# Optimization experiments

Measured on AMD Instinct MI355X. Metric: run time of the kernel, lower is better.

Reference implementation:

```python
import jax, jax.numpy as jnp
import numpy as np

B, N, C, H, L, FF, OUT = 8, 512, 1024, 16, 6, 4096, 2
HD = C // H
EPS = 1e-6


def _pos_encoding(n, d):
    pos = np.arange(n)[:, None].astype(np.float64)
    i = np.arange(d)[None, :].astype(np.float64)
    ang = pos / np.power(10000.0, 2 * (i // 2) / np.float32(d))
    ang[:, 0::2] = np.sin(ang[:, 0::2])
    ang[:, 1::2] = np.cos(ang[:, 1::2])
    return jnp.asarray(ang[None], dtype=jnp.float32)  # [1, N, C]


def setup_inputs() -> dict:
    key = jax.random.key(0)
    ks = jax.random.split(key, 16)
    s = 0.02
    inp = {
        'inputs': jax.random.normal(ks[0], (B, N, C), jnp.float32),
        'attention_mask': jnp.ones((B, 1, 1, N), jnp.int32),
        'pos_enc': _pos_encoding(N, C),
        'Wi': jax.random.normal(ks[1], (C, C), jnp.float32) * s,
        'bi': jnp.zeros((C,), jnp.float32),
        'ln1_g': jnp.ones((L, C), jnp.float32),
        'ln1_b': jnp.zeros((L, C), jnp.float32),
        'Wqkv': jax.random.normal(ks[2], (L, 3 * C, C), jnp.float32) * s,
        'bqkv': jnp.zeros((L, 3 * C), jnp.float32),
        'Wo': jax.random.normal(ks[3], (L, C, C), jnp.float32) * s,
        'bo': jnp.zeros((L, C), jnp.float32),
        'ln2_g': jnp.ones((L, C), jnp.float32),
        'ln2_b': jnp.zeros((L, C), jnp.float32),
        'W1': jax.random.normal(ks[4], (L, FF, C), jnp.float32) * s,
        'b1': jnp.zeros((L, FF), jnp.float32),
        'W2': jax.random.normal(ks[5], (L, C, FF), jnp.float32) * s,
        'b2': jnp.zeros((L, C), jnp.float32),
        'Wout': jax.random.normal(ks[6], (OUT, C), jnp.float32) * s,
        'bout': jnp.zeros((OUT,), jnp.float32),
    }
    return inp


def _layernorm(x, g, b):
    mu = jnp.mean(x, axis=-1, keepdims=True)
    var = jnp.mean(jnp.square(x - mu), axis=-1, keepdims=True)
    return (x - mu) * jax.lax.rsqrt(var + EPS) * g + b


def _forward(inputs, attention_mask, pos_enc, Wi, bi, ln1_g, ln1_b, Wqkv, bqkv,
             Wo, bo, ln2_g, ln2_b, W1, b1, W2, b2, Wout, bout):
    scale = HD ** -0.5
    x = inputs @ Wi.T + bi
    x = x + pos_enc
    for l in range(L):
        h = _layernorm(x, ln1_g[l], ln1_b[l])
        qkv = (h @ Wqkv[l].T + bqkv[l]).reshape(B, N, 3, H, HD)
        qkv = qkv.transpose(2, 0, 3, 1, 4)  # [3, B, H, N, HD]
        q, k, v = qkv[0], qkv[1], qkv[2]
        attn = jnp.einsum('bhqd,bhkd->bhqk', q, k) * scale
        attn = jnp.where(attention_mask == 0, jnp.float32(-1e9), attn)
        attn = jax.nn.softmax(attn, axis=-1)
        o = jnp.einsum('bhqk,bhkd->bhqd', attn, v)
        o = o.transpose(0, 2, 1, 3).reshape(B, N, C)
        x = x + (o @ Wo[l].T + bo[l])
        h = _layernorm(x, ln2_g[l], ln2_b[l])
        f = jax.nn.gelu(h @ W1[l].T + b1[l], approximate=False)
        x = x + (f @ W2[l].T + b2[l])
    return jax.nn.sigmoid(x @ Wout.T + bout)


def reference(inputs, attention_mask, pos_enc, Wi, bi, ln1_g, ln1_b, Wqkv, bqkv,
              Wo, bo, ln2_g, ln2_b, W1, b1, W2, b2, Wout, bout):
    return _forward(inputs, attention_mask, pos_enc, Wi, bi, ln1_g, ln1_b, Wqkv,
                    bqkv, Wo, bo, ln2_g, ln2_b, W1, b1, W2, b2, Wout, bout)
```

## Files before the change

### kernel.cpp

```cpp
#include <hip/hip_runtime.h>

typedef unsigned short u16;
typedef __bf16 bf16x8 __attribute__((ext_vector_type(8)));
typedef float f32x4 __attribute__((ext_vector_type(4)));
typedef u16 us8 __attribute__((ext_vector_type(8)));

__device__ __forceinline__ u16 f2bf(float f) {
    unsigned u = __float_as_uint(f);
    u += 0x7fffu + ((u >> 16) & 1u);
    return (u16)(u >> 16);
}
__device__ __forceinline__ float bf2f(u16 h) {
    return __uint_as_float(((unsigned)h) << 16);
}
__device__ __forceinline__ void async16(const void* g, void* l) {
    __builtin_amdgcn_global_load_lds((const __attribute__((address_space(1))) void*)g,
                                     (__attribute__((address_space(3))) void*)l, 16, 0, 0);
}

#define BM 128
#define BN 128
#define BK 32

enum { EPI_QKV = 0, EPI_XOUT = 1, EPI_GELU = 3, EPI_RAW = 4, EPI_PV = 5, EPI_ATOMIC = 6 };

template <int EPI>
__global__ __launch_bounds__(256, 4) void gemm_bt(
    const u16* __restrict__ A, int lda, long sAo, long sAi,
    const u16* __restrict__ B, int ldb, long sBo, long sBi,
    void* __restrict__ Cp, int ldc, long sCo, long sCi,
    const float* __restrict__ bias,
    int K, int innerB, int nStore,
    int gxt, int sm, int sn, int nSlabM)
{
    __shared__ __align__(16) u16 sA[BM * BK];
    __shared__ __align__(16) u16 sB[BN * BK];

    const int t = threadIdx.x;
    const int l = t & 63;
    const int w = t >> 6;

    const int pid = blockIdx.x;
    int tm, tn;
    if (sm > 0) {
        const int xcd = pid & 7, ii = pid >> 3;
        tm = (xcd % nSlabM) * sm + ii % sm;
        tn = (xcd / nSlabM) * sn + ii / sm;
    } else {
        tn = pid % gxt;
        tm = pid / gxt;
    }
    const int m0 = tm * BM;
    const int n0 = tn * BN;
    const int z = blockIdx.y;

    const u16 *Ab, *Bb;
    size_t cB;
    bool addb;
    if constexpr (EPI == EPI_ATOMIC) {
        Ab = A + (size_t)z * K;
        Bb = B + (size_t)z * K;
        cB = 0;
        addb = (z == 0);
    } else {
        const int zo = z / innerB, zi = z - zo * innerB;
        Ab = A + (size_t)zo * sAo + (size_t)zi * sAi;
        Bb = B + (size_t)zo * sBo + (size_t)zi * sBi;
        cB = (size_t)zo * sCo + (size_t)zi * sCi;
        addb = true;
    }

    const int sr = l >> 2;
    const int sp = l & 3;
    const int qg = (sp - ((sr >> 1) & 3)) & 3;

    const u16* gA0 = Ab + (size_t)(m0 + w * 32 + sr) * lda + qg * 8;
    const u16* gA1 = Ab + (size_t)(m0 + w * 32 + 16 + sr) * lda + qg * 8;
    const u16* gB0 = Bb + (size_t)(n0 + w * 32 + sr) * ldb + qg * 8;
    const u16* gB1 = Bb + (size_t)(n0 + w * 32 + 16 + sr) * ldb + qg * 8;
    u16* lA0 = sA + (w * 32) * BK;
    u16* lA1 = sA + (w * 32 + 16) * BK;
    u16* lB0 = sB + (w * 32) * BK;
    u16* lB1 = sB + (w * 32 + 16) * BK;

    const int wm = (w >> 1) * 64;
    const int wn = (w & 1) * 64;
    const int lm = l & 15;
    const int q = l >> 4;
    const int cp = ((q + ((lm >> 1) & 3)) & 3) * 8;

    int aOff[4], bOff[4];
#pragma unroll
    for (int i = 0; i < 4; ++i) {
        aOff[i] = (wm + i * 16 + lm) * BK + cp;
        bOff[i] = (wn + i * 16 + lm) * BK + cp;
    }

    f32x4 acc[4][4] = {};

    for (int kt = 0; kt < K; kt += BK) {
        __syncthreads();
        async16(gA0, lA0); async16(gA1, lA1);
        async16(gB0, lB0); async16(gB1, lB1);
        gA0 += BK; gA1 += BK; gB0 += BK; gB1 += BK;
        __syncthreads();

        us8 av[4], bv[4];
#pragma unroll
        for (int i = 0; i < 4; ++i) av[i] = *(const us8*)&sA[aOff[i]];
#pragma unroll
        for (int j = 0; j < 4; ++j) bv[j] = *(const us8*)&sB[bOff[j]];
#pragma unroll
        for (int i = 0; i < 4; ++i)
#pragma unroll
            for (int j = 0; j < 4; ++j)
                acc[i][j] = __builtin_amdgcn_mfma_f32_16x16x32_bf16(
                    __builtin_bit_cast(bf16x8, av[i]),
                    __builtin_bit_cast(bf16x8, bv[j]), acc[i][j], 0, 0, 0);
    }

    const int quad4 = q * 4;
#pragma unroll
    for (int j = 0; j < 4; ++j) {
        const int n = n0 + wn + j * 16 + lm;
        if (n >= nStore) continue;
        const float bb = (bias && addb) ? bias[n] : 0.0f;
#pragma unroll
        for (int i = 0; i < 4; ++i) {
#pragma unroll
            for (int r2 = 0; r2 < 4; ++r2) {
                const int m = m0 + wm + i * 16 + quad4 + r2;
                float v = acc[i][j][r2] + bb;
                if constexpr (EPI == EPI_GELU)
                    v = 0.5f * v * (1.0f + erff(v * 0.70710678118654752f));
                if constexpr (EPI == EPI_ATOMIC)
                    atomicAdd(&((float*)Cp)[cB + (size_t)m * ldc + n], v);
                else if constexpr (EPI == EPI_XOUT)
                    ((float*)Cp)[cB + (size_t)m * ldc + n] = v;
                else
                    ((u16*)Cp)[cB + (size_t)m * ldc + n] = f2bf(v);
            }
        }
    }
}

__global__ __launch_bounds__(256) void cast_k(const float* __restrict__ s,
                                              u16* __restrict__ d, int n8)
{
    int i = blockIdx.x * 256 + threadIdx.x;
    if (i >= n8) return;
    const float4* s4 = (const float4*)s;
    float4 a = s4[2 * i], b = s4[2 * i + 1];
    us8 o;
    o[0] = f2bf(a.x); o[1] = f2bf(a.y); o[2] = f2bf(a.z); o[3] = f2bf(a.w);
    o[4] = f2bf(b.x); o[5] = f2bf(b.y); o[6] = f2bf(b.z); o[7] = f2bf(b.w);
    *(us8*)(d + (size_t)i * 8) = o;
}

__global__ __launch_bounds__(256) void cast4_k(
    const float* __restrict__ s0, const float* __restrict__ s1,
    const float* __restrict__ s2, const float* __restrict__ s3,
    u16* __restrict__ d0, u16* __restrict__ d1,
    u16* __restrict__ d2, u16* __restrict__ d3)
{
    int i = blockIdx.x * 256 + threadIdx.x;
    const float* s; u16* d; int off;
    if (i < 393216)       { s = s0; d = d0; off = i; }
    else if (i < 524288)  { s = s1; d = d1; off = i - 393216; }
    else if (i < 1048576) { s = s2; d = d2; off = i - 524288; }
    else                  { s = s3; d = d3; off = i - 1048576; }
    const float4* s4 = (const float4*)s;
    float4 a = s4[2 * off], b = s4[2 * off + 1];
    us8 o;
    o[0] = f2bf(a.x); o[1] = f2bf(a.y); o[2] = f2bf(a.z); o[3] = f2bf(a.w);
    o[4] = f2bf(b.x); o[5] = f2bf(b.y); o[6] = f2bf(b.z); o[7] = f2bf(b.w);
    *(us8*)(d + (size_t)off * 8) = o;
}

__global__ __launch_bounds__(256) void add_pos_k(float* __restrict__ x,
                                                 const float* __restrict__ pos)
{
    int i = blockIdx.x * 256 + threadIdx.x;
    int m = i >> 8;
    int c = i & 255;
    float4 pv = ((const float4*)pos)[((m & 511) << 8) + c];
    float4 v = ((float4*)x)[i];
    v.x += pv.x; v.y += pv.y; v.z += pv.z; v.w += pv.w;
    ((float4*)x)[i] = v;
}

__global__ __launch_bounds__(256) void ln_k(const float* __restrict__ x,
                                            const float* __restrict__ g,
                                            const float* __restrict__ b,
                                            u16* __restrict__ h)
{
    const int row = blockIdx.x;
    const int t = threadIdx.x;
    const float4 v = ((const float4*)(x + (size_t)row * 1024))[t];
    float s = v.x + v.y + v.z + v.w;
    float ss = v.x * v.x + v.y * v.y + v.z * v.z + v.w * v.w;
#pragma unroll
    for (int o = 32; o >= 1; o >>= 1) {
        s += __shfl_xor(s, o);
        ss += __shfl_xor(ss, o);
    }
    __shared__ float rs[4], rss[4];
    if ((t & 63) == 0) { rs[t >> 6] = s; rss[t >> 6] = ss; }
    __syncthreads();
    s = rs[0] + rs[1] + rs[2] + rs[3];
    ss = rss[0] + rss[1] + rss[2] + rss[3];
    const float mean = s * (1.0f / 1024.0f);
    const float var = ss * (1.0f / 1024.0f) - mean * mean;
    const float rstd = rsqrtf(var + 1e-6f);
    const float4 gv = ((const float4*)g)[t];
    const float4 bv = ((const float4*)b)[t];
    ushort4 o4;
    o4.x = f2bf((v.x - mean) * rstd * gv.x + bv.x);
    o4.y = f2bf((v.y - mean) * rstd * gv.y + bv.y);
    o4.z = f2bf((v.z - mean) * rstd * gv.z + bv.z);
    o4.w = f2bf((v.w - mean) * rstd * gv.w + bv.w);
    ((ushort4*)(h + (size_t)row * 1024))[t] = o4;
}

__global__ __launch_bounds__(256) void softmax_k(u16* __restrict__ S)
{
    int wv = blockIdx.x * 4 + (threadIdx.x >> 6);
    int l = threadIdx.x & 63;
    u16* row = S + (size_t)wv * 512 + l * 8;
    us8 v = *(const us8*)row;
    float f[8];
    float mx = -1e30f;
#pragma unroll
    for (int j = 0; j < 8; ++j) { f[j] = bf2f(v[j]) * 0.125f; mx = fmaxf(mx, f[j]); }
#pragma unroll
    for (int o = 32; o >= 1; o >>= 1) mx = fmaxf(mx, __shfl_xor(mx, o));
    float sm = 0.0f;
#pragma unroll
    for (int j = 0; j < 8; ++j) { f[j] = __expf(f[j] - mx); sm += f[j]; }
#pragma unroll
    for (int o = 32; o >= 1; o >>= 1) sm += __shfl_xor(sm, o);
    const float inv = 1.0f / sm;
    us8 ov;
#pragma unroll
    for (int j = 0; j < 8; ++j) ov[j] = f2bf(f[j] * inv);
    *(us8*)row = ov;
}

__global__ __launch_bounds__(256) void transpose_v_k(const u16* __restrict__ qkv,
                                                     u16* __restrict__ Vt)
{
    __shared__ __align__(16) u16 T[64 * 72];
    const int t = threadIdx.x;
    const int nt = blockIdx.x;
    const int z = blockIdx.y;
    const int b = z >> 4, h = z & 15;
    const int rr = t >> 3;
    const int cc = (t & 7) * 8;
#pragma unroll
    for (int rep = 0; rep < 2; ++rep) {
        int n_loc = rep * 32 + rr;
        const u16* src = qkv + (size_t)(b * 512 + nt * 64 + n_loc) * 3072 + 2048 + h * 64 + cc;
        *(us8*)&T[n_loc * 72 + cc] = *(const us8*)src;
    }
    __syncthreads();
#pragma unroll
    for (int rep = 0; rep < 2; ++rep) {
        int d_loc = rep * 32 + rr;
        us8 v;
#pragma unroll
        for (int jj = 0; jj < 8; ++jj) v[jj] = T[(cc + jj) * 72 + d_loc];
        *(us8*)(Vt + (size_t)z * 65536 + (size_t)d_loc * 512 + nt * 64 + cc) = v;
    }
}

__global__ __launch_bounds__(256) void final_k(const float* __restrict__ x,
                                               const float* __restrict__ Wout,
                                               const float* __restrict__ bout,
                                               float* __restrict__ out)
{
    int row = blockIdx.x * 4 + (threadIdx.x >> 6);
    int l = threadIdx.x & 63;
    const float4* xr = (const float4*)(x + (size_t)row * 1024);
    const float4* w0 = (const float4*)Wout;
    const float4* w1 = (const float4*)(Wout + 1024);
    float d0 = 0.0f, d1 = 0.0f;
#pragma unroll
    for (int jj = 0; jj < 4; ++jj) {
        float4 v = xr[l + jj * 64];
        float4 a = w0[l + jj * 64];
        float4 b = w1[l + jj * 64];
        d0 += v.x * a.x + v.y * a.y + v.z * a.z + v.w * a.w;
        d1 += v.x * b.x + v.y * b.y + v.z * b.z + v.w * b.w;
    }
#pragma unroll
    for (int o = 32; o >= 1; o >>= 1) { d0 += __shfl_xor(d0, o); d1 += __shfl_xor(d1, o); }
    if (l == 0) {
        out[(size_t)row * 2 + 0] = 1.0f / (1.0f + __expf(-(d0 + bout[0])));
        out[(size_t)row * 2 + 1] = 1.0f / (1.0f + __expf(-(d1 + bout[1])));
    }
}

extern "C" void kernel_launch(void* const* d_in, const int* in_sizes, int n_in,
                              void* d_out, int out_size, void* d_ws, size_t ws_size,
                              hipStream_t stream)
{
    (void)in_sizes; (void)n_in; (void)out_size;
    const float* inputs = (const float*)d_in[0];
    const float* pos  = (const float*)d_in[2];
    const float* Wi   = (const float*)d_in[3];
    const float* bi   = (const float*)d_in[4];
    const float* ln1g = (const float*)d_in[5];
    const float* ln1b = (const float*)d_in[6];
    const float* Wqkv = (const float*)d_in[7];
    const float* bqkv = (const float*)d_in[8];
    const float* Wo   = (const float*)d_in[9];
    const float* bo   = (const float*)d_in[10];
    const float* ln2g = (const float*)d_in[11];
    const float* ln2b = (const float*)d_in[12];
    const float* W1   = (const float*)d_in[13];
    const float* b1   = (const float*)d_in[14];
    const float* W2   = (const float*)d_in[15];
    const float* b2   = (const float*)d_in[16];
    const float* Wout = (const float*)d_in[17];
    const float* bout = (const float*)d_in[18];
    float* out = (float*)d_out;

    char* p = (char*)d_ws;
    auto alloc = [&](size_t n) -> void* {
        void* r = (void*)p;
        p += (n + 255) & ~(size_t)255;
        return r;
    };
    u16* wWi_   = (u16*)alloc(1048576ull * 2);
    u16* wQKVl  = (u16*)alloc(3145728ull * 2);
    u16* wWol   = (u16*)alloc(1048576ull * 2);
    u16* wW1l   = (u16*)alloc(4194304ull * 2);
    u16* wW2l   = (u16*)alloc(4194304ull * 2);
    float* x    = (float*)alloc(4194304ull * 4);
    u16* h_bf   = (u16*)alloc(4194304ull * 2);
    u16* qkv_bf = (u16*)alloc(12582912ull * 2);
    u16* S_bf   = (u16*)alloc(33554432ull * 2);
    u16* Vt     = (u16*)alloc(8388608ull * 2);
    u16* io_bf  = (u16*)alloc(4194304ull * 2);
    if ((size_t)(p - (char*)d_ws) > ws_size) return;

    const dim3 blk(256);

    cast_k<<<2048, blk, 0, stream>>>(inputs, io_bf, 524288);
    cast_k<<<512, blk, 0, stream>>>(Wi, wWi_, 131072);

    gemm_bt<EPI_XOUT><<<dim3(256, 1), blk, 0, stream>>>(
        io_bf, 1024, 0, 0, wWi_, 1024, 0, 0, x, 1024, 0, 0,
        bi, 1024, 1, 1024, 8, 16, 2, 2);
    add_pos_k<<<4096, blk, 0, stream>>>(x, pos);

    hipMemsetAsync(Vt, 0, 8388608ull * 2, stream);

    for (int l = 0; l < 6; ++l) {
        cast4_k<<<6144, blk, 0, stream>>>(
            Wqkv + (size_t)l * 3145728, Wo + (size_t)l * 1048576,
            W1 + (size_t)l * 4194304, W2 + (size_t)l * 4194304,
            wQKVl, wWol, wW1l, wW2l);

        ln_k<<<4096, blk, 0, stream>>>(x, ln1g + l * 1024, ln1b + l * 1024, h_bf);
        gemm_bt<EPI_QKV><<<dim3(768, 1), blk, 0, stream>>>(
            h_bf, 1024, 0, 0, wQKVl, 1024, 0, 0, qkv_bf, 3072, 0, 0,
            bqkv + l * 3072, 1024, 1, 3072, 24, 16, 6, 2);

        transpose_v_k<<<dim3(8, 128), blk, 0, stream>>>(qkv_bf, Vt);

        gemm_bt<EPI_RAW><<<dim3(16, 128), blk, 0, stream>>>(
            qkv_bf, 3072, 512ll * 3072, 64,
            qkv_bf + 1024, 3072, 512ll * 3072, 64,
            S_bf, 512, 16ll * 262144, 262144,
            nullptr, 64, 16, 512, 4, 0, 0, 0);
        softmax_k<<<16384, blk, 0, stream>>>(S_bf);

        gemm_bt<EPI_PV><<<dim3(4, 128), blk, 0, stream>>>(
            S_bf, 512, 16ll * 262144, 262144,
            Vt, 512, 16ll * 65536, 65536,
            io_bf, 1024, 512ll * 1024, 64,
            nullptr, 512, 16, 64, 1, 0, 0, 0);

        gemm_bt<EPI_ATOMIC><<<dim3(256, 2), blk, 0, stream>>>(
            io_bf, 1024, 0, 0, wWol, 1024, 0, 0, x, 1024, 0, 0,
            bo + l * 1024, 512, 1, 1024, 8, 16, 2, 2);

        ln_k<<<4096, blk, 0, stream>>>(x, ln2g + l * 1024, ln2b + l * 1024, h_bf);
        gemm_bt<EPI_GELU><<<dim3(1024, 1), blk, 0, stream>>>(
            h_bf, 1024, 0, 0, wW1l, 1024, 0, 0, S_bf , 4096, 0, 0,
            b1 + l * 4096, 1024, 1, 4096, 32, 16, 8, 2);
        gemm_bt<EPI_ATOMIC><<<dim3(256, 2), blk, 0, stream>>>(
            S_bf, 4096, 0, 0, wW2l, 4096, 0, 0, x, 1024, 0, 0,
            b2 + l * 1024, 2048, 1, 1024, 8, 16, 2, 2);
    }

    final_k<<<1024, blk, 0, stream>>>(x, Wout, bout, out);
}
```

Measured before the change: 2.101 ms.

## Fuse attention into flash kernel and double-buffer GEMM LDS tiles

Replaces the three-step attention (QK^T GEMM writing a full score matrix, separate softmax, PV GEMM) with a fused flash-attention kernel using online softmax. Scores stay in registers and LDS instead of round-tripping a 64MB bf16 buffer through HBM. Separately, the generic GEMM gains double-buffered LDS with prefetch of the next K tile, which removes one barrier per iteration but doubles LDS use and may lower occupancy. The batched-stride parameters and the Vt memset are dropped.

```diff
diff --git a/kernel.cpp b/kernel.cpp
--- a/kernel.cpp
+++ b/kernel.cpp
@@ -22,19 +22,19 @@
 #define BN 128
 #define BK 32
 
-enum { EPI_QKV = 0, EPI_XOUT = 1, EPI_GELU = 3, EPI_RAW = 4, EPI_PV = 5, EPI_ATOMIC = 6 };
+enum { EPI_QKV = 0, EPI_XOUT = 1, EPI_GELU = 3, EPI_ATOMIC = 6 };
 
 template <int EPI>
 __global__ __launch_bounds__(256, 4) void gemm_bt(
-    const u16* __restrict__ A, int lda, long sAo, long sAi,
-    const u16* __restrict__ B, int ldb, long sBo, long sBi,
-    void* __restrict__ Cp, int ldc, long sCo, long sCi,
+    const u16* __restrict__ A, int lda,
+    const u16* __restrict__ B, int ldb,
+    void* __restrict__ Cp, int ldc,
     const float* __restrict__ bias,
-    int K, int innerB, int nStore,
+    int K, int nStore,
     int gxt, int sm, int sn, int nSlabM)
 {
-    __shared__ __align__(16) u16 sA[BM * BK];
-    __shared__ __align__(16) u16 sB[BN * BK];
+    __shared__ __align__(16) u16 sA[2][BM * BK];
+    __shared__ __align__(16) u16 sB[2][BN * BK];
 
     const int t = threadIdx.x;
     const int l = t & 63;
@@ -55,20 +55,9 @@
     const int z = blockIdx.y;
 
     const u16 *Ab, *Bb;
-    size_t cB;
-    bool addb;
-    if constexpr (EPI == EPI_ATOMIC) {
-        Ab = A + (size_t)z * K;
-        Bb = B + (size_t)z * K;
-        cB = 0;
-        addb = (z == 0);
-    } else {
-        const int zo = z / innerB, zi = z - zo * innerB;
-        Ab = A + (size_t)zo * sAo + (size_t)zi * sAi;
-        Bb = B + (size_t)zo * sBo + (size_t)zi * sBi;
-        cB = (size_t)zo * sCo + (size_t)zi * sCi;
-        addb = true;
-    }
+    bool addb = true;
+    if constexpr (EPI == EPI_ATOMIC) { Ab = A + (size_t)z * K; Bb = B + (size_t)z * K; addb = (z == 0); }
+    else { Ab = A; Bb = B; }
 
     const int sr = l >> 2;
     const int sp = l & 3;
@@ -78,10 +67,7 @@
     const u16* gA1 = Ab + (size_t)(m0 + w * 32 + 16 + sr) * lda + qg * 8;
     const u16* gB0 = Bb + (size_t)(n0 + w * 32 + sr) * ldb + qg * 8;
     const u16* gB1 = Bb + (size_t)(n0 + w * 32 + 16 + sr) * ldb + qg * 8;
-    u16* lA0 = sA + (w * 32) * BK;
-    u16* lA1 = sA + (w * 32 + 16) * BK;
-    u16* lB0 = sB + (w * 32) * BK;
-    u16* lB1 = sB + (w * 32 + 16) * BK;
+    const int dA0 = (w * 32) * BK, dA1 = (w * 32 + 16) * BK;
 
     const int wm = (w >> 1) * 64;
     const int wn = (w & 1) * 64;
@@ -98,18 +84,24 @@
 
     f32x4 acc[4][4] = {};
 
+    async16(gA0, &sA[0][dA0]); async16(gA1, &sA[0][dA1]);
+    async16(gB0, &sB[0][dA0]); async16(gB1, &sB[0][dA1]);
+    gA0 += BK; gA1 += BK; gB0 += BK; gB1 += BK;
+
+    int cur = 0;
     for (int kt = 0; kt < K; kt += BK) {
         __syncthreads();
-        async16(gA0, lA0); async16(gA1, lA1);
-        async16(gB0, lB0); async16(gB1, lB1);
-        gA0 += BK; gA1 += BK; gB0 += BK; gB1 += BK;
-        __syncthreads();
-
+        if (kt + BK < K) {
+            const int nx = cur ^ 1;
+            async16(gA0, &sA[nx][dA0]); async16(gA1, &sA[nx][dA1]);
+            async16(gB0, &sB[nx][dA0]); async16(gB1, &sB[nx][dA1]);
+            gA0 += BK; gA1 += BK; gB0 += BK; gB1 += BK;
+        }
         us8 av[4], bv[4];
 #pragma unroll
-        for (int i = 0; i < 4; ++i) av[i] = *(const us8*)&sA[aOff[i]];
-#pragma unroll
-        for (int j = 0; j < 4; ++j) bv[j] = *(const us8*)&sB[bOff[j]];
+        for (int i = 0; i < 4; ++i) av[i] = *(const us8*)&sA[cur][aOff[i]];
+#pragma unroll
+        for (int j = 0; j < 4; ++j) bv[j] = *(const us8*)&sB[cur][bOff[j]];
 #pragma unroll
         for (int i = 0; i < 4; ++i)
 #pragma unroll
@@ -117,6 +109,7 @@
                 acc[i][j] = __builtin_amdgcn_mfma_f32_16x16x32_bf16(
                     __builtin_bit_cast(bf16x8, av[i]),
                     __builtin_bit_cast(bf16x8, bv[j]), acc[i][j], 0, 0, 0);
+        cur ^= 1;
     }
 
     const int quad4 = q * 4;
@@ -134,14 +127,172 @@
                 if constexpr (EPI == EPI_GELU)
                     v = 0.5f * v * (1.0f + erff(v * 0.70710678118654752f));
                 if constexpr (EPI == EPI_ATOMIC)
-                    atomicAdd(&((float*)Cp)[cB + (size_t)m * ldc + n], v);
+                    atomicAdd(&((float*)Cp)[(size_t)m * ldc + n], v);
                 else if constexpr (EPI == EPI_XOUT)
-                    ((float*)Cp)[cB + (size_t)m * ldc + n] = v;
+                    ((float*)Cp)[(size_t)m * ldc + n] = v;
                 else
-                    ((u16*)Cp)[cB + (size_t)m * ldc + n] = f2bf(v);
+                    ((u16*)Cp)[(size_t)m * ldc + n] = f2bf(v);
             }
         }
     }
+}
+
+__global__ __launch_bounds__(256, 2) void flash_k(
+    const u16* __restrict__ qkv, const u16* __restrict__ Vt,
+    u16* __restrict__ O)
+{
+    __shared__ __align__(16) u16 smem[32768];
+    u16* sQ = smem;
+    u16* sP = smem;
+    u16* sK = smem + 16384;
+    u16* sV = smem + 24576;
+
+    const int t = threadIdx.x;
+    const int l = t & 63;
+    const int w = t >> 6;
+    const int lm = l & 15;
+    const int quad = l >> 4;
+    const int z = blockIdx.y;
+    const int b = z >> 4, h = z & 15;
+    const int q0 = blockIdx.x * 128;
+
+    const size_t rowQ = (size_t)(b * 512 + q0) * 3072 + h * 64;
+#pragma unroll
+    for (int s = 0; s < 4; ++s) {
+        const int slot = s * 256 + t;
+        const int r = slot >> 3, pp = slot & 7;
+        const int c = (pp - r) & 7;
+        async16(qkv + rowQ + (size_t)r * 3072 + c * 8, sQ + slot * 8);
+    }
+    __syncthreads();
+
+    us8 qf[2][2];
+#pragma unroll
+    for (int i = 0; i < 2; ++i)
+#pragma unroll
+        for (int kc = 0; kc < 2; ++kc) {
+            const int row = 32 * w + i * 16 + lm;
+            const int p = (kc * 4 + quad + row) & 7;
+            qf[i][kc] = *(const us8*)&sQ[row * 64 + p * 8];
+        }
+
+    f32x4 Oa[2][4] = {};
+    float mrow[2][4], lrow[2][4];
+#pragma unroll
+    for (int i = 0; i < 2; ++i)
+#pragma unroll
+        for (int r2 = 0; r2 < 4; ++r2) { mrow[i][r2] = -1e30f; lrow[i][r2] = 0.0f; }
+
+    for (int j = 0; j < 4; ++j) {
+        __syncthreads();
+        const size_t rowK = (size_t)(b * 512 + j * 128) * 3072 + 1024 + h * 64;
+#pragma unroll
+        for (int s = 0; s < 4; ++s) {
+            const int slot = s * 256 + t;
+            const int r = slot >> 3, pp = slot & 7;
+            const int c = (pp - r) & 7;
+            async16(qkv + rowK + (size_t)r * 3072 + c * 8, sK + slot * 8);
+        }
+        const size_t baseV = (size_t)z * 65536 + j * 128;
+#pragma unroll
+        for (int s = 0; s < 4; ++s) {
+            const int slot = s * 256 + t;
+            const int r = slot >> 4, pp = slot & 15;
+            const int c = (pp - r) & 15;
+            async16(Vt + baseV + (size_t)r * 512 + c * 8, sV + slot * 8);
+        }
+        __syncthreads();
+
+        f32x4 S[2][8] = {};
+#pragma unroll
+        for (int kc = 0; kc < 2; ++kc)
+#pragma unroll
+            for (int n = 0; n < 8; ++n) {
+                const int rowb = n * 16 + lm;
+                const int p = (kc * 4 + quad + rowb) & 7;
+                const us8 kf = *(const us8*)&sK[rowb * 64 + p * 8];
+#pragma unroll
+                for (int i = 0; i < 2; ++i)
+                    S[i][n] = __builtin_amdgcn_mfma_f32_16x16x32_bf16(
+                        __builtin_bit_cast(bf16x8, qf[i][kc]),
+                        __builtin_bit_cast(bf16x8, kf), S[i][n], 0, 0, 0);
+            }
+
+        float alpha[2][4], mnew[2][4];
+#pragma unroll
+        for (int i = 0; i < 2; ++i)
+#pragma unroll
+            for (int r2 = 0; r2 < 4; ++r2) {
+                float mx = -1e30f;
+#pragma unroll
+                for (int n = 0; n < 8; ++n) {
+                    S[i][n][r2] *= 0.125f;
+                    mx = fmaxf(mx, S[i][n][r2]);
+                }
+#pragma unroll
+                for (int o = 8; o >= 1; o >>= 1) mx = fmaxf(mx, __shfl_xor(mx, o));
+                mnew[i][r2] = fmaxf(mrow[i][r2], mx);
+                alpha[i][r2] = __expf(mrow[i][r2] - mnew[i][r2]);
+                mrow[i][r2] = mnew[i][r2];
+            }
+#pragma unroll
+        for (int i = 0; i < 2; ++i)
+#pragma unroll
+            for (int r2 = 0; r2 < 4; ++r2) {
+                float sum = 0.0f;
+                const int row = 32 * w + i * 16 + quad * 4 + r2;
+#pragma unroll
+                for (int n = 0; n < 8; ++n) {
+                    const float pv = __expf(S[i][n][r2] - mnew[i][r2]);
+                    sum += pv;
+                    const int col = n * 16 + lm;
+                    const int p = ((col >> 3) + row) & 15;
+                    sP[row * 128 + p * 8 + (col & 7)] = f2bf(pv);
+                }
+#pragma unroll
+                for (int o = 8; o >= 1; o >>= 1) sum += __shfl_xor(sum, o);
+                lrow[i][r2] = alpha[i][r2] * lrow[i][r2] + sum;
+            }
+#pragma unroll
+        for (int i = 0; i < 2; ++i)
+#pragma unroll
+            for (int n = 0; n < 4; ++n)
+#pragma unroll
+                for (int r2 = 0; r2 < 4; ++r2) Oa[i][n][r2] *= alpha[i][r2];
+
+#pragma unroll
+        for (int kc = 0; kc < 4; ++kc) {
+            us8 pf[2];
+#pragma unroll
+            for (int i = 0; i < 2; ++i) {
+                const int row = 32 * w + i * 16 + lm;
+                const int p = (kc * 4 + quad + row) & 15;
+                pf[i] = *(const us8*)&sP[row * 128 + p * 8];
+            }
+#pragma unroll
+            for (int n = 0; n < 4; ++n) {
+                const int rowb = n * 16 + lm;
+                const int p = (kc * 4 + quad + rowb) & 15;
+                const us8 vf = *(const us8*)&sV[rowb * 128 + p * 8];
+#pragma unroll
+                for (int i = 0; i < 2; ++i)
+                    Oa[i][n] = __builtin_amdgcn_mfma_f32_16x16x32_bf16(
+                        __builtin_bit_cast(bf16x8, pf[i]),
+                        __builtin_bit_cast(bf16x8, vf), Oa[i][n], 0, 0, 0);
+            }
+        }
+    }
+
+#pragma unroll
+    for (int i = 0; i < 2; ++i)
+#pragma unroll
+        for (int r2 = 0; r2 < 4; ++r2) {
+            const float inv = 1.0f / lrow[i][r2];
+            const int g = b * 512 + q0 + 32 * w + i * 16 + quad * 4 + r2;
+#pragma unroll
+            for (int n = 0; n < 4; ++n)
+                O[(size_t)g * 1024 + h * 64 + n * 16 + lm] = f2bf(Oa[i][n][r2] * inv);
+        }
 }
 
 __global__ __launch_bounds__(256) void cast_k(const float* __restrict__ s,
@@ -220,30 +371,6 @@
     o4.z = f2bf((v.z - mean) * rstd * gv.z + bv.z);
     o4.w = f2bf((v.w - mean) * rstd * gv.w + bv.w);
     ((ushort4*)(h + (size_t)row * 1024))[t] = o4;
-}
-
-__global__ __launch_bounds__(256) void softmax_k(u16* __restrict__ S)
-{
-    int wv = blockIdx.x * 4 + (threadIdx.x >> 6);
-    int l = threadIdx.x & 63;
-    u16* row = S + (size_t)wv * 512 + l * 8;
-    us8 v = *(const us8*)row;
-    float f[8];
-    float mx = -1e30f;
-#pragma unroll
-    for (int j = 0; j < 8; ++j) { f[j] = bf2f(v[j]) * 0.125f; mx = fmaxf(mx, f[j]); }
-#pragma unroll
-    for (int o = 32; o >= 1; o >>= 1) mx = fmaxf(mx, __shfl_xor(mx, o));
-    float sm = 0.0f;
-#pragma unroll
-    for (int j = 0; j < 8; ++j) { f[j] = __expf(f[j] - mx); sm += f[j]; }
-#pragma unroll
-    for (int o = 32; o >= 1; o >>= 1) sm += __shfl_xor(sm, o);
-    const float inv = 1.0f / sm;
-    us8 ov;
-#pragma unroll
-    for (int j = 0; j < 8; ++j) ov[j] = f2bf(f[j] * inv);
-    *(us8*)row = ov;
 }
 
 __global__ __launch_bounds__(256) void transpose_v_k(const u16* __restrict__ qkv,
@@ -339,7 +466,7 @@
     float* x    = (float*)alloc(4194304ull * 4);
     u16* h_bf   = (u16*)alloc(4194304ull * 2);
     u16* qkv_bf = (u16*)alloc(12582912ull * 2);
-    u16* S_bf   = (u16*)alloc(33554432ull * 2);
+    u16* f_bf   = (u16*)alloc(16777216ull * 2);
     u16* Vt     = (u16*)alloc(8388608ull * 2);
     u16* io_bf  = (u16*)alloc(4194304ull * 2);
     if ((size_t)(p - (char*)d_ws) > ws_size) return;
@@ -350,11 +477,9 @@
     cast_k<<<512, blk, 0, stream>>>(Wi, wWi_, 131072);
 
     gemm_bt<EPI_XOUT><<<dim3(256, 1), blk, 0, stream>>>(
-        io_bf, 1024, 0, 0, wWi_, 1024, 0, 0, x, 1024, 0, 0,
-        bi, 1024, 1, 1024, 8, 16, 2, 2);
+        io_bf, 1024, wWi_, 1024, x, 1024,
+        bi, 1024, 1024, 8, 16, 2, 2);
     add_pos_k<<<4096, blk, 0, stream>>>(x, pos);
-
-    hipMemsetAsync(Vt, 0, 8388608ull * 2, stream);
 
     for (int l = 0; l < 6; ++l) {
         cast4_k<<<6144, blk, 0, stream>>>(
@@ -364,35 +489,24 @@
 
         ln_k<<<4096, blk, 0, stream>>>(x, ln1g + l * 1024, ln1b + l * 1024, h_bf);
         gemm_bt<EPI_QKV><<<dim3(768, 1), blk, 0, stream>>>(
-            h_bf, 1024, 0, 0, wQKVl, 1024, 0, 0, qkv_bf, 3072, 0, 0,
-            bqkv + l * 3072, 1024, 1, 3072, 24, 16, 6, 2);
+            h_bf, 1024, wQKVl, 1024, qkv_bf, 3072,
+            bqkv + l * 3072, 1024, 3072, 24, 16, 6, 2);
 
         transpose_v_k<<<dim3(8, 128), blk, 0, stream>>>(qkv_bf, Vt);
 
-        gemm_bt<EPI_RAW><<<dim3(16, 128), blk, 0, stream>>>(
-            qkv_bf, 3072, 512ll * 3072, 64,
-            qkv_bf + 1024, 3072, 512ll * 3072, 64,
-            S_bf, 512, 16ll * 262144, 262144,
-            nullptr, 64, 16, 512, 4, 0, 0, 0);
-        softmax_k<<<16384, blk, 0, stream>>>(S_bf);
-
-        gemm_bt<EPI_PV><<<dim3(4, 128), blk, 0, stream>>>(
-            S_bf, 512, 16ll * 262144, 262144,
-            Vt, 512, 16ll * 65536, 65536,
-            io_bf, 1024, 512ll * 1024, 64,
-            nullptr, 512, 16, 64, 1, 0, 0, 0);
+        flash_k<<<dim3(4, 128), blk, 0, stream>>>(qkv_bf, Vt, io_bf);
 
         gemm_bt<EPI_ATOMIC><<<dim3(256, 2), blk, 0, stream>>>(
-            io_bf, 1024, 0, 0, wWol, 1024, 0, 0, x, 1024, 0, 0,
-            bo + l * 1024, 512, 1, 1024, 8, 16, 2, 2);
+            io_bf, 1024, wWol, 1024, x, 1024,
+            bo + l * 1024, 512, 1024, 8, 16, 2, 2);
 
         ln_k<<<4096, blk, 0, stream>>>(x, ln2g + l * 1024, ln2b + l * 1024, h_bf);
         gemm_bt<EPI_GELU><<<dim3(1024, 1), blk, 0, stream>>>(
-            h_bf, 1024, 0, 0, wW1l, 1024, 0, 0, S_bf , 4096, 0, 0,
-            b1 + l * 4096, 1024, 1, 4096, 32, 16, 8, 2);
+            h_bf, 1024, wW1l, 1024, f_bf, 4096,
+            b1 + l * 4096, 1024, 4096, 32, 16, 8, 2);
         gemm_bt<EPI_ATOMIC><<<dim3(256, 2), blk, 0, stream>>>(
-            S_bf, 4096, 0, 0, wW2l, 4096, 0, 0, x, 1024, 0, 0,
-            b2 + l * 1024, 2048, 1, 1024, 8, 16, 2, 2);
+            f_bf, 4096, wW2l, 4096, x, 1024,
+            b2 + l * 1024, 2048, 1024, 8, 16, 2, 2);
     }
 
     final_k<<<1024, blk, 0, stream>>>(x, Wout, bout, out);
```

New measurement: 1.810 ms. -13.8%, faster.
